# Performance work log

Measured on AMD Instinct MI355X. Metric: run time of the kernel, lower is better.

The kernel has to match this reference:

```python
import jax, jax.numpy as jnp
import numpy as np


def setup_inputs() -> dict:
    key = jax.random.key(0)
    k1, k2 = jax.random.split(key)
    d, T, n = 256, 8192, 64
    # scale down so exp(ht^T D^T D hj) stays in range, as typical trained D would
    H = jax.random.normal(k1, (d, T), dtype=jnp.float32) * 0.1
    D = jax.random.normal(k2, (n, d), dtype=jnp.float32) * 0.1
    l2 = jnp.ones((), dtype=jnp.float32)
    return {"H": H, "D": D, "l2": l2}


def reference(H, D, l2):
    # H: [d, T], D: [n, d]
    DH = D @ H                                   # [n, T] = D @ H_T.T
    # S[t, j] = h_t^T (D^T D) h_j  == (DH)^T (DH)
    S = jnp.einsum('nt,nj->tj', DH, DH)          # [T, T]
    # beta_j = exp(-0.5 * ||D h_j||^2); row t: attn[t,:] = beta * exp(S[t,:]) / sum
    log_beta = -0.5 * jnp.sum(DH * DH, axis=0)   # [T]
    attn_map = jax.nn.softmax(S + log_beta[None, :], axis=1)  # [T, T]
    Z = l2 * (H @ attn_map)                      # [d, T]
    return Z
```

## Files before the change

kernel.cpp:

```cpp
#include <hip/hip_runtime.h>

#define T_DIM 8192
#define D_DIM 256
#define N_DIM 64
#define LOG2E 1.44269504f

typedef __bf16 bf16x8 __attribute__((ext_vector_type(8)));
typedef __bf16 bf16x4 __attribute__((ext_vector_type(4)));
typedef float f32x16 __attribute__((ext_vector_type(16)));

__device__ __forceinline__ f32x16 zero16() {
  f32x16 v;
#pragma unroll
  for (int i = 0; i < 16; ++i) v[i] = 0.f;
  return v;
}


__global__ __launch_bounds__(256) void k_dh(const float* __restrict__ H,
                                            const float* __restrict__ Dm,
                                            __bf16* __restrict__ DHf,
                                            float* __restrict__ lbe,
                                            float* __restrict__ rowsum) {
  __shared__ __bf16 HlThi[64 * 264];
  __shared__ __bf16 HlTlo[64 * 264];
  __shared__ __bf16 DHs[64 * 72];
  const int tid = threadIdx.x;
  const int t0 = blockIdx.x * 64;
  const int lane = tid & 63;
  const int wave = tid >> 6;
  const int h = lane >> 5;
  const int l31 = lane & 31;
  const float4* H4 = (const float4*)H;
#pragma unroll
  for (int r = 0; r < 16; ++r) {
    int idx = r * 256 + tid;
    int d = idx >> 4, tc = idx & 15;
    float4 v = H4[(size_t)d * (T_DIM / 4) + (t0 >> 2) + tc];
    float vv[4] = {v.x, v.y, v.z, v.w};
#pragma unroll
    for (int i = 0; i < 4; ++i) {
      __bf16 hi = (__bf16)vv[i];
      float lo = vv[i] - (float)hi;
      HlThi[(tc * 4 + i) * 264 + d] = hi;
      HlTlo[(tc * 4 + i) * 264 + d] = (__bf16)lo;
    }
  }
  __syncthreads();
  const int tt = wave & 1, nh = wave >> 1;
  const int m = tt * 32 + l31;
  const int n = nh * 32 + l31;
  f32x16 c = zero16();
  for (int kk = 0; kk < 16; ++kk) {
    bf16x8 ahi = *(const bf16x8*)&HlThi[m * 264 + kk * 16 + h * 8];
    bf16x8 alo = *(const bf16x8*)&HlTlo[m * 264 + kk * 16 + h * 8];
    const float4* dp = (const float4*)(Dm + (size_t)n * 256 + kk * 16 + h * 8);
    float4 b0 = dp[0], b1 = dp[1];
    float bv[8] = {b0.x, b0.y, b0.z, b0.w, b1.x, b1.y, b1.z, b1.w};
    bf16x8 bhi, blo;
#pragma unroll
    for (int i = 0; i < 8; ++i) {
      __bf16 hi = (__bf16)bv[i];
      bhi[i] = hi;
      blo[i] = (__bf16)(bv[i] - (float)hi);
    }
    c = __builtin_amdgcn_mfma_f32_32x32x16_bf16(ahi, bhi, c, 0, 0, 0);
    c = __builtin_amdgcn_mfma_f32_32x32x16_bf16(ahi, blo, c, 0, 0, 0);
    c = __builtin_amdgcn_mfma_f32_32x32x16_bf16(alo, bhi, c, 0, 0, 0);
  }
#pragma unroll
  for (int r = 0; r < 16; ++r) {
    int row = tt * 32 + (r & 3) + 8 * (r >> 2) + 4 * h;
    DHs[row * 72 + n] = (__bf16)c[r];
  }
  __syncthreads();
#pragma unroll
  for (int r = 0; r < 2; ++r) {
    int idx = r * 256 + tid;
    int g = idx >> 8, cc = (idx >> 5) & 7, l = idx & 31;
    bf16x8 w = *(const bf16x8*)&DHs[(g * 32 + l) * 72 + cc * 8];
    *(bf16x8*)(DHf + (size_t)(blockIdx.x * 2 + g) * 2048 + cc * 256 + l * 8) = w;
  }
  if (tid < 64) {
    float s = 0.f;
#pragma unroll
    for (int q = 0; q < 8; ++q) {
      bf16x8 w = *(const bf16x8*)&DHs[tid * 72 + q * 8];
#pragma unroll
      for (int i = 0; i < 8; ++i) { float f = (float)w[i]; s += f * f; }
    }
    lbe[t0 + tid] = -0.5f * s * LOG2E;
    rowsum[t0 + tid] = 0.f;
  }
}

__global__ __launch_bounds__(512, 4) void k_rowsum(const __bf16* __restrict__ DHf,
                                                   const float* __restrict__ lbe,
                                                   float* __restrict__ rowsum) {
  __shared__ float red2[256][33];
  const int tid = threadIdx.x;
  const int lane = tid & 63;
  const int wave = tid >> 6;
  const int h = lane >> 5;
  const int l31 = lane & 31;
  const int t0 = (int)(blockIdx.x >> 4) * 256;
  const int jbase = (int)(blockIdx.x & 15) * 512;
  const size_t Gt = (size_t)(t0 >> 5) + wave;
  const size_t Gj0 = (size_t)(jbase >> 5);
  bf16x8 aR[4];
#pragma unroll
  for (int kk = 0; kk < 4; ++kk)
    aR[kk] = *(const bf16x8*)(DHf + Gt * 2048 + kk * 512 + lane * 8);
  float racc[16];
#pragma unroll
  for (int r = 0; r < 16; ++r) racc[r] = 0.f;
  bf16x8 b0[4], b1[4];
#pragma unroll
  for (int kk = 0; kk < 4; ++kk) {
    b0[kk] = *(const bf16x8*)(DHf + Gj0 * 2048 + kk * 512 + lane * 8);
    b1[kk] = *(const bf16x8*)(DHf + (Gj0 + 1) * 2048 + kk * 512 + lane * 8);
  }
#pragma unroll
  for (int jj = 0; jj < 8; ++jj) {
    {
      const float lbv = lbe[jbase + (jj * 2) * 32 + l31];
      f32x16 s0 = zero16(), s1 = zero16();
      s0 = __builtin_amdgcn_mfma_f32_32x32x16_bf16(aR[0], b0[0], s0, 0, 0, 0);
      s1 = __builtin_amdgcn_mfma_f32_32x32x16_bf16(aR[1], b0[1], s1, 0, 0, 0);
      s0 = __builtin_amdgcn_mfma_f32_32x32x16_bf16(aR[2], b0[2], s0, 0, 0, 0);
      s1 = __builtin_amdgcn_mfma_f32_32x32x16_bf16(aR[3], b0[3], s1, 0, 0, 0);
      if (jj < 7) {
        const size_t Gj = Gj0 + jj * 2 + 2;
#pragma unroll
        for (int kk = 0; kk < 4; ++kk)
          b0[kk] = *(const bf16x8*)(DHf + Gj * 2048 + kk * 512 + lane * 8);
      }
#pragma unroll
      for (int r = 0; r < 16; ++r)
        racc[r] += __builtin_amdgcn_exp2f(
            __builtin_fmaf(s0[r] + s1[r], LOG2E, lbv));
    }
    {
      const float lbv = lbe[jbase + (jj * 2 + 1) * 32 + l31];
      f32x16 s0 = zero16(), s1 = zero16();
      s0 = __builtin_amdgcn_mfma_f32_32x32x16_bf16(aR[0], b1[0], s0, 0, 0, 0);
      s1 = __builtin_amdgcn_mfma_f32_32x32x16_bf16(aR[1], b1[1], s1, 0, 0, 0);
      s0 = __builtin_amdgcn_mfma_f32_32x32x16_bf16(aR[2], b1[2], s0, 0, 0, 0);
      s1 = __builtin_amdgcn_mfma_f32_32x32x16_bf16(aR[3], b1[3], s1, 0, 0, 0);
      if (jj < 7) {
        const size_t Gj = Gj0 + jj * 2 + 3;
#pragma unroll
        for (int kk = 0; kk < 4; ++kk)
          b1[kk] = *(const bf16x8*)(DHf + Gj * 2048 + kk * 512 + lane * 8);
      }
#pragma unroll
      for (int r = 0; r < 16; ++r)
        racc[r] += __builtin_amdgcn_exp2f(
            __builtin_fmaf(s0[r] + s1[r], LOG2E, lbv));
    }
  }
#pragma unroll
  for (int r = 0; r < 16; ++r) {
    int tl = wave * 32 + (r & 3) + 8 * (r >> 2) + 4 * h;
    red2[tl][l31] = racc[r];
  }
  __syncthreads();
  if (tid < 256) {
    float s = 0.f;
#pragma unroll 8
    for (int c = 0; c < 32; ++c) s += red2[tid][c];
    atomicAdd(&rowsum[t0 + tid], s);
  }
}

__global__ __launch_bounds__(256) void k_scaleH(const float* __restrict__ H,
                                                const float* __restrict__ rowsum,
                                                __bf16* __restrict__ Hbf_sw) {
  __shared__ float rinvL[64];
  const int tid = threadIdx.x;
  const int bx = blockIdx.x;
  const int tblk = bx >> 1, dh = bx & 1;
  const int t0 = tblk * 64;
  if (tid < 64) rinvL[tid] = 1.0f / rowsum[t0 + tid];
  __syncthreads();
#pragma unroll
  for (int itr = 0; itr < 4; ++itr) {
    int idx = itr * 256 + tid;
    int dl = idx >> 3, tbp = idx & 7;
    int d = dh * 128 + dl;
    int swz = (d ^ (d >> 3)) & 7;
    int tloc = (tbp ^ swz) << 3;
    const float4* hp = (const float4*)(H + (size_t)d * T_DIM + t0 + tloc);
    float4 v0 = hp[0], v1 = hp[1];
    float4 r0 = *(const float4*)&rinvL[tloc];
    float4 r1 = *(const float4*)&rinvL[tloc + 4];
    bf16x8 w;
    w[0] = (__bf16)(v0.x * r0.x); w[1] = (__bf16)(v0.y * r0.y);
    w[2] = (__bf16)(v0.z * r0.z); w[3] = (__bf16)(v0.w * r0.w);
    w[4] = (__bf16)(v1.x * r1.x); w[5] = (__bf16)(v1.y * r1.y);
    w[6] = (__bf16)(v1.z * r1.z); w[7] = (__bf16)(v1.w * r1.w);
    *(bf16x8*)(Hbf_sw + (size_t)tblk * 16384 + (size_t)d * 64 + tbp * 8) = w;
  }
}

__global__ __launch_bounds__(256, 2) void k_z(const __bf16* __restrict__ Hbf_sw,
                                              const __bf16* __restrict__ DHf,
                                              const float* __restrict__ lbe,
                                              float* __restrict__ Zp) {
  __shared__ __bf16 Hs[2][128 * 64];
  __shared__ __bf16 Pt[2][128 * 64];
  const int tid = threadIdx.x;
  const int lane = tid & 63;
  const int wave = tid >> 6;
  const int h = lane >> 5;
  const int l31 = lane & 31;
  const int bx = blockIdx.x;
  const int ts = bx & 3;
  const int dh = (bx >> 2) & 1;
  const int j0 = (bx >> 3) * 128;
  const int s_tt = wave & 1, s_jg = wave >> 1;
  bf16x8 bS[2][4];
  float lbv[2];
#pragma unroll
  for (int q = 0; q < 2; ++q) {
    const size_t Gj = (j0 >> 5) + s_jg * 2 + q;
#pragma unroll
    for (int kk = 0; kk < 4; ++kk)
      bS[q][kk] = *(const bf16x8*)(DHf + Gj * 2048 + kk * 512 + lane * 8);
    lbv[q] = lbe[j0 + (s_jg * 2 + q) * 32 + l31];
  }
  f32x16 acc[2][2];
#pragma unroll
  for (int u = 0; u < 2; ++u)
#pragma unroll
    for (int v = 0; v < 2; ++v) acc[u][v] = zero16();

#define DMA_HS(buf_, it_)                                                       \
  {                                                                             \
    const __bf16* gsrc =                                                        \
        Hbf_sw + (size_t)(ts * 32 + (it_)) * 16384 + (size_t)dh * 8192;         \
    _Pragma("unroll") for (int r = 0; r < 4; ++r) {                             \
      int chunk = wave * 4 + r;                                                 \
      __builtin_amdgcn_global_load_lds(                                         \
          (const __attribute__((address_space(1))) unsigned int*)(gsrc +        \
              chunk * 512 + lane * 8),                                          \
          (__attribute__((address_space(3))) unsigned int*)(&Hs[buf_][0] +      \
              chunk * 512),                                                     \
          16, 0, 0);                                                            \
    }                                                                           \
  }

#define LOAD_AR(reg_, n_)                                                       \
  {                                                                             \
    const size_t Gt_ = (size_t)(ts * 64 + (n_)*2 + s_tt);                       \
    _Pragma("unroll") for (int kk = 0; kk < 4; ++kk)                            \
        (reg_)[kk] = *(const bf16x8*)(DHf + Gt_ * 2048 + kk * 512 + lane * 8);  \
  }

#define S_PHASE(p_, reg_)                                                       \
  {                                                                             \
    _Pragma("unroll") for (int q = 0; q < 2; ++q) {                             \
      f32x16 s = zero16();                                                      \
      _Pragma("unroll") for (int kk = 0; kk < 4; ++kk)                          \
          s = __builtin_amdgcn_mfma_f32_32x32x16_bf16((reg_)[kk], bS[q][kk], s, \
                                                      0, 0, 0);                 \
      const int jl = (s_jg * 2 + q) * 32 + l31;                                 \
      const int sj = (jl ^ (jl >> 3)) & 7;                                      \
      _Pragma("unroll") for (int g = 0; g < 4; ++g) {                           \
        const int tl = s_tt * 32 + g * 8 + 4 * h;                               \
        bf16x4 pv;                                                              \
        pv[0] = (__bf16)__builtin_amdgcn_exp2f(                                 \
            __builtin_fmaf(s[g * 4 + 0], LOG2E, lbv[q]));                       \
        pv[1] = (__bf16)__builtin_amdgcn_exp2f(                                 \
            __builtin_fmaf(s[g * 4 + 1], LOG2E, lbv[q]));                       \
        pv[2] = (__bf16)__builtin_amdgcn_exp2f(                                 \
            __builtin_fmaf(s[g * 4 + 2], LOG2E, lbv[q]));                       \
        pv[3] = (__bf16)__builtin_amdgcn_exp2f(                                 \
            __builtin_fmaf(s[g * 4 + 3], LOG2E, lbv[q]));                       \
        const int cchunk = tl >> 3;                                             \
        *(bf16x4*)&Pt[p_][jl * 64 + ((cchunk ^ sj) << 3) + 4 * h] = pv;         \
      }                                                                         \
    }                                                                           \
  }

#define Z_PHASE(p_)                                                             \
  {                                                                             \
    __builtin_amdgcn_s_setprio(1);                                              \
    _Pragma("unroll") for (int kk = 0; kk < 4; ++kk) {                          \
      const int c = kk * 2 + h;                                                 \
      bf16x8 af[2], bw[2];                                                      \
      _Pragma("unroll") for (int u = 0; u < 2; ++u) {                           \
        int dl = (wave & 1) * 64 + u * 32 + l31;                                \
        af[u] =                                                                 \
            *(const bf16x8*)&Hs[p_][dl * 64 + ((c ^ ((dl ^ (dl >> 3)) & 7)) << 3)]; \
      }                                                                         \
      _Pragma("unroll") for (int v = 0; v < 2; ++v) {                           \
        int j = (wave >> 1) * 64 + v * 32 + l31;                                \
        bw[v] =                                                                 \
            *(const bf16x8*)&Pt[p_][j * 64 + ((c ^ ((j ^ (j >> 3)) & 7)) << 3)]; \
      }                                                                         \
      _Pragma("unroll") for (int u = 0; u < 2; ++u)                             \
          _Pragma("unroll") for (int v = 0; v < 2; ++v)                         \
              acc[u][v] = __builtin_amdgcn_mfma_f32_32x32x16_bf16(              \
                  af[u], bw[v], acc[u][v], 0, 0, 0);                            \
    }                                                                           \
    __builtin_amdgcn_s_setprio(0);                                              \
  }

  bf16x8 aR[4], aRn[4];
  LOAD_AR(aR, 0);
  DMA_HS(0, 0);
  S_PHASE(0, aR);
  LOAD_AR(aRn, 1);
  __syncthreads();

  for (int ii = 0; ii < 16; ++ii) {
    const int it0 = ii * 2;
    DMA_HS(1, it0 + 1);
    if (it0 < 30) LOAD_AR(aR, it0 + 2);
    S_PHASE(1, aRn);
    Z_PHASE(0);
    __syncthreads();
    if (it0 + 1 < 31) {
      DMA_HS(0, it0 + 2);
      S_PHASE(0, aR);
    }
    if (it0 + 1 < 30) LOAD_AR(aRn, it0 + 3);
    Z_PHASE(1);
    __syncthreads();
  }
#undef Z_PHASE
#undef S_PHASE
#undef LOAD_AR
#undef DMA_HS
  float* zp = Zp + (size_t)ts * (256 * (size_t)T_DIM);
#pragma unroll
  for (int u = 0; u < 2; ++u)
#pragma unroll
    for (int v = 0; v < 2; ++v)
#pragma unroll
      for (int r = 0; r < 16; ++r) {
        int d = dh * 128 + (wave & 1) * 64 + u * 32 + (r & 3) + 8 * (r >> 2) + 4 * h;
        int j = j0 + (wave >> 1) * 64 + v * 32 + l31;
        zp[(size_t)d * T_DIM + j] = acc[u][v][r];
      }
}

__global__ __launch_bounds__(256) void k_zred(const float* __restrict__ Zp,
                                              const float* __restrict__ l2p,
                                              float* __restrict__ Z) {
  const int i = blockIdx.x * 256 + threadIdx.x;
  const float l2v = l2p[0];
  const float4* zp4 = (const float4*)Zp;
  float4 a = zp4[i];
#pragma unroll
  for (int s = 1; s < 4; ++s) {
    float4 b = zp4[(size_t)s * 524288 + i];
    a.x += b.x; a.y += b.y; a.z += b.z; a.w += b.w;
  }
  float4 o = {a.x * l2v, a.y * l2v, a.z * l2v, a.w * l2v};
  ((float4*)Z)[i] = o;
}

extern "C" void kernel_launch(void* const* d_in, const int* in_sizes, int n_in,
                              void* d_out, int out_size, void* d_ws,
                              size_t ws_size, hipStream_t stream) {
  (void)in_sizes; (void)n_in; (void)out_size; (void)ws_size;
  const float* H = (const float*)d_in[0];
  const float* Dm = (const float*)d_in[1];
  const float* l2 = (const float*)d_in[2];
  float* Z = (float*)d_out;
  char* ws = (char*)d_ws;
  __bf16* DHf = (__bf16*)ws;
  float* lbe = (float*)(ws + 1048576);
  float* rowsum = (float*)(ws + 1048576 + 32768);
  __bf16* Hbf_sw = (__bf16*)(ws + 1114112);
  float* Zp = (float*)(ws + 5308416);

  k_dh<<<128, 256, 0, stream>>>(H, Dm, DHf, lbe, rowsum);
  k_rowsum<<<512, 512, 0, stream>>>(DHf, lbe, rowsum);
  k_scaleH<<<256, 256, 0, stream>>>(H, rowsum, Hbf_sw);
  k_z<<<512, 256, 0, stream>>>(Hbf_sw, DHf, lbe, Zp);
  k_zred<<<2048, 256, 0, stream>>>(Zp, l2, Z);
}
```

Before: 147.0 us.

## Split k_z work across eight waves per block instead of four

Doubles k_z's block size to 512 threads (8 waves), so each wave computes one 32-column S tile and one 64x32 Z accumulator pair instead of two of each. The H tile DMA is spread across more waves, and the per-wave register footprint shrinks (bS, acc halved), with launch bounds raised to 4 blocks per CU. This aims at more latency hiding and better occupancy, at the cost of more waves taking part in each barrier and less per-wave MFMA reuse of the A fragments.

```diff
diff --git a/kernel.cpp b/kernel.cpp
--- a/kernel.cpp
+++ b/kernel.cpp
@@ -203,7 +203,7 @@
   }
 }
 
-__global__ __launch_bounds__(256, 2) void k_z(const __bf16* __restrict__ Hbf_sw,
+__global__ __launch_bounds__(512, 4) void k_z(const __bf16* __restrict__ Hbf_sw,
                                               const __bf16* __restrict__ DHf,
                                               const float* __restrict__ lbe,
                                               float* __restrict__ Zp) {
@@ -219,28 +219,26 @@
   const int dh = (bx >> 2) & 1;
   const int j0 = (bx >> 3) * 128;
   const int s_tt = wave & 1, s_jg = wave >> 1;
-  bf16x8 bS[2][4];
-  float lbv[2];
-#pragma unroll
-  for (int q = 0; q < 2; ++q) {
-    const size_t Gj = (j0 >> 5) + s_jg * 2 + q;
+  const int dq = wave & 1, jv = wave >> 1;
+  bf16x8 bS[4];
+  float lbv;
+  {
+    const size_t Gj = (size_t)(j0 >> 5) + s_jg;
 #pragma unroll
     for (int kk = 0; kk < 4; ++kk)
-      bS[q][kk] = *(const bf16x8*)(DHf + Gj * 2048 + kk * 512 + lane * 8);
-    lbv[q] = lbe[j0 + (s_jg * 2 + q) * 32 + l31];
-  }
-  f32x16 acc[2][2];
-#pragma unroll
-  for (int u = 0; u < 2; ++u)
-#pragma unroll
-    for (int v = 0; v < 2; ++v) acc[u][v] = zero16();
+      bS[kk] = *(const bf16x8*)(DHf + Gj * 2048 + kk * 512 + lane * 8);
+    lbv = lbe[j0 + s_jg * 32 + l31];
+  }
+  f32x16 acc[2];
+#pragma unroll
+  for (int u = 0; u < 2; ++u) acc[u] = zero16();
 
 #define DMA_HS(buf_, it_)                                                       \
   {                                                                             \
     const __bf16* gsrc =                                                        \
         Hbf_sw + (size_t)(ts * 32 + (it_)) * 16384 + (size_t)dh * 8192;         \
-    _Pragma("unroll") for (int r = 0; r < 4; ++r) {                             \
-      int chunk = wave * 4 + r;                                                 \
+    _Pragma("unroll") for (int r = 0; r < 2; ++r) {                             \
+      int chunk = wave * 2 + r;                                                 \
       __builtin_amdgcn_global_load_lds(                                         \
           (const __attribute__((address_space(1))) unsigned int*)(gsrc +        \
               chunk * 512 + lane * 8),                                          \
@@ -259,27 +257,26 @@
 
 #define S_PHASE(p_, reg_)                                                       \
   {                                                                             \
-    _Pragma("unroll") for (int q = 0; q < 2; ++q) {                             \
-      f32x16 s = zero16();                                                      \
-      _Pragma("unroll") for (int kk = 0; kk < 4; ++kk)                          \
-          s = __builtin_amdgcn_mfma_f32_32x32x16_bf16((reg_)[kk], bS[q][kk], s, \
-                                                      0, 0, 0);                 \
-      const int jl = (s_jg * 2 + q) * 32 + l31;                                 \
-      const int sj = (jl ^ (jl >> 3)) & 7;                                      \
-      _Pragma("unroll") for (int g = 0; g < 4; ++g) {                           \
-        const int tl = s_tt * 32 + g * 8 + 4 * h;                               \
-        bf16x4 pv;                                                              \
-        pv[0] = (__bf16)__builtin_amdgcn_exp2f(                                 \
-            __builtin_fmaf(s[g * 4 + 0], LOG2E, lbv[q]));                       \
-        pv[1] = (__bf16)__builtin_amdgcn_exp2f(                                 \
-            __builtin_fmaf(s[g * 4 + 1], LOG2E, lbv[q]));                       \
-        pv[2] = (__bf16)__builtin_amdgcn_exp2f(                                 \
-            __builtin_fmaf(s[g * 4 + 2], LOG2E, lbv[q]));                       \
-        pv[3] = (__bf16)__builtin_amdgcn_exp2f(                                 \
-            __builtin_fmaf(s[g * 4 + 3], LOG2E, lbv[q]));                       \
-        const int cchunk = tl >> 3;                                             \
-        *(bf16x4*)&Pt[p_][jl * 64 + ((cchunk ^ sj) << 3) + 4 * h] = pv;         \
-      }                                                                         \
+    f32x16 s = zero16();                                                        \
+    s = __builtin_amdgcn_mfma_f32_32x32x16_bf16((reg_)[0], bS[0], s, 0, 0, 0);  \
+    s = __builtin_amdgcn_mfma_f32_32x32x16_bf16((reg_)[1], bS[1], s, 0, 0, 0);  \
+    s = __builtin_amdgcn_mfma_f32_32x32x16_bf16((reg_)[2], bS[2], s, 0, 0, 0);  \
+    s = __builtin_amdgcn_mfma_f32_32x32x16_bf16((reg_)[3], bS[3], s, 0, 0, 0);  \
+    const int jl = s_jg * 32 + l31;                                             \
+    const int sj = (jl ^ (jl >> 3)) & 7;                                        \
+    _Pragma("unroll") for (int g = 0; g < 4; ++g) {                             \
+      const int tl = s_tt * 32 + g * 8 + 4 * h;                                 \
+      bf16x4 pv;                                                                \
+      pv[0] = (__bf16)__builtin_amdgcn_exp2f(                                   \
+          __builtin_fmaf(s[g * 4 + 0], LOG2E, lbv));                            \
+      pv[1] = (__bf16)__builtin_amdgcn_exp2f(                                   \
+          __builtin_fmaf(s[g * 4 + 1], LOG2E, lbv));                            \
+      pv[2] = (__bf16)__builtin_amdgcn_exp2f(                                   \
+          __builtin_fmaf(s[g * 4 + 2], LOG2E, lbv));                            \
+      pv[3] = (__bf16)__builtin_amdgcn_exp2f(                                   \
+          __builtin_fmaf(s[g * 4 + 3], LOG2E, lbv));                            \
+      const int cchunk = tl >> 3;                                               \
+      *(bf16x4*)&Pt[p_][jl * 64 + ((cchunk ^ sj) << 3) + 4 * h] = pv;           \
     }                                                                           \
   }
 
@@ -288,21 +285,19 @@
     __builtin_amdgcn_s_setprio(1);                                              \
     _Pragma("unroll") for (int kk = 0; kk < 4; ++kk) {                          \
       const int c = kk * 2 + h;                                                 \
-      bf16x8 af[2], bw[2];                                                      \
+      bf16x8 af[2], bw;                                                         \
       _Pragma("unroll") for (int u = 0; u < 2; ++u) {                           \
-        int dl = (wave & 1) * 64 + u * 32 + l31;                                \
+        int dl = dq * 64 + u * 32 + l31;                                        \
         af[u] =                                                                 \
             *(const bf16x8*)&Hs[p_][dl * 64 + ((c ^ ((dl ^ (dl >> 3)) & 7)) << 3)]; \
       }                                                                         \
-      _Pragma("unroll") for (int v = 0; v < 2; ++v) {                           \
-        int j = (wave >> 1) * 64 + v * 32 + l31;                                \
-        bw[v] =                                                                 \
-            *(const bf16x8*)&Pt[p_][j * 64 + ((c ^ ((j ^ (j >> 3)) & 7)) << 3)]; \
+      {                                                                         \
+        int j = jv * 32 + l31;                                                  \
+        bw = *(const bf16x8*)&Pt[p_][j * 64 + ((c ^ ((j ^ (j >> 3)) & 7)) << 3)]; \
       }                                                                         \
       _Pragma("unroll") for (int u = 0; u < 2; ++u)                             \
-          _Pragma("unroll") for (int v = 0; v < 2; ++v)                         \
-              acc[u][v] = __builtin_amdgcn_mfma_f32_32x32x16_bf16(              \
-                  af[u], bw[v], acc[u][v], 0, 0, 0);                            \
+          acc[u] = __builtin_amdgcn_mfma_f32_32x32x16_bf16(af[u], bw, acc[u],   \
+                                                           0, 0, 0);            \
     }                                                                           \
     __builtin_amdgcn_s_setprio(0);                                              \
   }
@@ -337,13 +332,11 @@
 #pragma unroll
   for (int u = 0; u < 2; ++u)
 #pragma unroll
-    for (int v = 0; v < 2; ++v)
-#pragma unroll
-      for (int r = 0; r < 16; ++r) {
-        int d = dh * 128 + (wave & 1) * 64 + u * 32 + (r & 3) + 8 * (r >> 2) + 4 * h;
-        int j = j0 + (wave >> 1) * 64 + v * 32 + l31;
-        zp[(size_t)d * T_DIM + j] = acc[u][v][r];
-      }
+    for (int r = 0; r < 16; ++r) {
+      int d = dh * 128 + dq * 64 + u * 32 + (r & 3) + 8 * (r >> 2) + 4 * h;
+      int j = j0 + jv * 32 + l31;
+      zp[(size_t)d * T_DIM + j] = acc[u][r];
+    }
 }
 
 __global__ __launch_bounds__(256) void k_zred(const float* __restrict__ Zp,
@@ -380,6 +373,6 @@
   k_dh<<<128, 256, 0, stream>>>(H, Dm, DHf, lbe, rowsum);
   k_rowsum<<<512, 512, 0, stream>>>(DHf, lbe, rowsum);
   k_scaleH<<<256, 256, 0, stream>>>(H, rowsum, Hbf_sw);
-  k_z<<<512, 256, 0, stream>>>(Hbf_sw, DHf, lbe, Zp);
+  k_z<<<512, 512, 0, stream>>>(Hbf_sw, DHf, lbe, Zp);
   k_zred<<<2048, 256, 0, stream>>>(Zp, l2, Z);
 }
```

New measurement: 148.4 us. No clear change (+0.9%).
